# Performance work log

Hardware: AMD Instinct MI355X
Metric: run time of the kernel (lower is better)

Reference implementation:

```python
import jax, jax.numpy as jnp
import numpy as np

N = 50000      # nodes
K = 16         # out-degree before symmetrization
B = 8          # graphs in batch
H = 384        # hidden_channels
D = 64         # padded max neighbor slots per node (degree ~2K avg, Poisson tail << 64)
E = 2 * N * K  # directed edges after symmetrization


def setup_inputs() -> dict:
    key = jax.random.key(0)
    k1, k2, k3, k4, k5 = jax.random.split(key, 5)
    per = N // B
    rng = np.random.default_rng(0)
    src = np.repeat(np.arange(N, dtype=np.int32), K)
    # destinations stay inside the same graph block so clusters never cross graphs
    dst = ((src // per) * per + rng.integers(0, per, size=N * K)).astype(np.int32)
    ei = np.stack([np.concatenate([src, dst]), np.concatenate([dst, src])])
    edge_index = jnp.asarray(ei, dtype=jnp.int32)
    h = jax.random.normal(k1, (N, H), jnp.float32)
    edge_weight = jax.random.uniform(k2, (E,), jnp.float32)
    batch = jnp.asarray(np.arange(N) // per, dtype=jnp.int32)
    bound = 1.0 / np.sqrt(H)
    W_rel = jax.random.uniform(k3, (H, H), jnp.float32, -bound, bound)
    b_rel = jax.random.uniform(k4, (H,), jnp.float32, -bound, bound)
    W_root = jax.random.uniform(k5, (H, H), jnp.float32, -bound, bound)
    return dict(h=h, edge_index=edge_index, edge_weight=edge_weight, batch=batch,
                W_rel=W_rel, b_rel=b_rel, W_root=W_root)


def _graclus(edge_index, edge_weight, n):
    """Deterministic greedy weighted matching (graclus). Nodes processed in
    index order; an unmatched node grabs its max-weight unmatched neighbor.
    Returns cluster id per node (= index of the lower-id node of each pair)."""
    src, dst = edge_index[0], edge_index[1]
    e = src.shape[0]
    order = jnp.argsort(src)  # stable sort by source node
    s, d, w = src[order], dst[order], edge_weight[order]
    start = jnp.searchsorted(s, jnp.arange(n, dtype=s.dtype))  # first edge of each node
    pos = jnp.arange(e, dtype=s.dtype) - start[s]               # slot within node's list
    nbrs = jnp.full((n, D), -1, dtype=s.dtype).at[s, pos].set(d, mode='drop')
    wts = jnp.full((n, D), -jnp.inf, dtype=w.dtype).at[s, pos].set(w, mode='drop')

    def body(u, state):
        cluster, matched = state
        nb = nbrs[u]
        cand = (nb >= 0) & (nb != u) & (~matched[nb])
        wv = jnp.where(cand, wts[u], -jnp.inf)
        j = jnp.argmax(wv)
        can_match = cand[j] & (~matched[u])
        v = jnp.where(can_match, nb[j], u)
        cluster = cluster.at[v].set(jnp.where(can_match, u, cluster[v]))
        matched = matched.at[u].set(True).at[v].set(True)
        return cluster, matched

    cluster0 = jnp.arange(n, dtype=jnp.int32)
    matched0 = jnp.zeros(n, dtype=bool)
    cluster, _ = jax.lax.fori_loop(0, n, body, (cluster0, matched0))
    return cluster


def _forward(h, edge_index, edge_weight, batch, W_rel, b_rel, W_root):
    n = h.shape[0]
    cluster = _graclus(edge_index, edge_weight, n)
    # consecutive relabeling (PyG consecutive_cluster); padded to n clusters
    is_rep = jnp.zeros(n, bool).at[cluster].set(True)
    new_id = jnp.cumsum(is_rep.astype(jnp.int32)) - 1
    c = new_id[cluster]                       # [n] cluster id in [0, num_clusters)
    count = jax.ops.segment_sum(jnp.ones(n, jnp.float32), c, num_segments=n)
    nonempty = count > 0
    # max_pool node features
    x = jax.ops.segment_max(h, c, num_segments=n)
    x = jnp.where(nonempty[:, None], x, 0.0)
    # pooled batch vector
    b_pool = jax.ops.segment_max(batch, c, num_segments=n)
    b_pool = jnp.where(nonempty, b_pool, 0)
    # pool_edge: relabel, drop self-loops, coalesce duplicates
    cs, cd = c[edge_index[0]], c[edge_index[1]]
    order = jnp.lexsort((cd, cs))
    cs_s, cd_s = cs[order], cd[order]
    first = jnp.concatenate([jnp.ones(1, bool), (cs_s[1:] != cs_s[:-1]) | (cd_s[1:] != cd_s[:-1])])
    keep = first & (cs_s != cd_s)
    # GraphConv: out = lin_rel(sum_j x_j) + lin_root(x), then activation
    msg = jnp.where(keep[:, None], x[cs_s], 0.0)
    aggr = jax.ops.segment_sum(msg, cd_s, num_segments=n)
    out = jax.nn.relu(aggr @ W_rel.T + b_rel + x @ W_root.T)
    out = jnp.where(nonempty[:, None], out, 0.0)  # zero padded cluster rows
    return out, b_pool


def reference(h, edge_index, edge_weight, batch, W_rel, b_rel, W_root):
    return _forward(h, edge_index, edge_weight, batch, W_rel, b_rel, W_root)
```

## Files before the change

kernel.cpp:

```cpp
#include <hip/hip_runtime.h>
#include <math.h>

#define NN 50000
#define HH 384
#define KKC 16
#define PER 6250
#define EE 1600000
#define NKE 800000

#define OFF_NBRS   0UL
#define OFF_WTS    12800000UL
#define OFF_ADJ    0UL
#define OFF_CNT2   25600000UL
#define OFF_ADJC   25800000UL
#define OFF_CLUS   26000000UL
#define OFF_MATE   26200000UL
#define OFF_NEWID  26400000UL
#define OFF_CMAP   26600000UL
#define OFF_REPOF  26800000UL
#define OFF_NC     27000000UL
#define OFF_AGGR   27000256UL

__global__ void k0_init(int* cnt2, int* adjcnt) {
    int i = blockIdx.x * blockDim.x + threadIdx.x;
    if (i < NN) { cnt2[i] = 0; adjcnt[i] = 0; }
}

__global__ void k1_build(const int* __restrict__ ei, const float* __restrict__ ew,
                         int* __restrict__ nbrs, float* __restrict__ wts) {
    int id = blockIdx.x * blockDim.x + threadIdx.x;
    if (id >= NN * 64) return;
    int slot = id & 63;
    int u = id >> 6;
    if (slot < KKC) {
        int e = u * KKC + slot;
        nbrs[id] = ei[EE + e];
        wts[id]  = ew[e];
    } else {
        nbrs[id] = -1;
        wts[id]  = -INFINITY;
    }
}

__global__ void k2_scatter(const int* __restrict__ ei, int* __restrict__ cnt2,
                           int* __restrict__ nbrs) {
    int i = blockIdx.x * blockDim.x + threadIdx.x;
    if (i >= NKE) return;
    int u = ei[EE + i];
    int slot = atomicAdd(&cnt2[u], 1);
    if (slot < 48) nbrs[u * 64 + 16 + slot] = i;
}

__global__ __launch_bounds__(256) void k3_rank(const int* __restrict__ cnt2,
                                               const float* __restrict__ ew,
                                               int* __restrict__ nbrs,
                                               float* __restrict__ wts) {
    int gid = blockIdx.x * blockDim.x + threadIdx.x;
    int u = gid >> 6;
    int lane = gid & 63;
    if (u >= NN) return;
    int cnt = cnt2[u]; if (cnt > 48) cnt = 48;
    int myi = (lane < cnt) ? nbrs[u * 64 + 16 + lane] : 0x7FFFFFFF;
    int rank = 0;
    for (int m = 0; m < cnt; ++m) {
        int ov = __shfl(myi, m, 64);
        if (lane < cnt && m != lane && ov < myi) rank++;
    }
    if (lane < cnt) {
        nbrs[u * 64 + 16 + rank] = myi >> 4;
        wts [u * 64 + 16 + rank] = ew[NKE + myi];
    }
}

#define DPPMAX(x, ctrl) fmaxf((x), __int_as_float(__builtin_amdgcn_update_dpp( \
        (int)0xFF800000, __float_as_int(x), (ctrl), 0xf, 0xf, false)))

__device__ __forceinline__ void gstep(int u, int nl, float wt, unsigned gw, unsigned hw,
                                      int lane, unsigned* mbits, int* clus, int* mt,
                                      int& v1, int& v2, int& v3) {
    bool um = (((hw >> (u & 31)) & 1u) != 0u) || (u == v1) || (u == v2) || (u == v3);
    int vnew = -1;
    if (!um) {
        bool cand = (nl > u) && !((gw >> (nl & 31)) & 1u)
                    && (nl != v1) && (nl != v2) && (nl != v3);
        unsigned long long bal = __ballot(cand);
        if (bal) {
            float wv = cand ? wt : -INFINITY;
            float m = wv;
            m = DPPMAX(m, 0x111);
            m = DPPMAX(m, 0x112);
            m = DPPMAX(m, 0x114);
            m = DPPMAX(m, 0x118);
            m = DPPMAX(m, 0x142);
            m = DPPMAX(m, 0x143);
            float wmax = __int_as_float(__builtin_amdgcn_readlane(__float_as_int(m), 63));
            unsigned long long em = __ballot(cand && (wv == wmax));
            int j = (int)__builtin_ctzll(em);
            int vl = __builtin_amdgcn_readlane(nl, j);
            if (lane == 0) {
                atomicOr(&mbits[u  >> 5], 1u << (u  & 31));
                atomicOr(&mbits[vl >> 5], 1u << (vl & 31));
                mt[u] = vl; mt[vl] = u; clus[vl] = u;
            }
            vnew = vl;
        } else {
            if (lane == 0) atomicOr(&mbits[u >> 5], 1u << (u & 31));
        }
    }
    v3 = v2; v2 = v1; v1 = vnew;
}

__global__ __launch_bounds__(64) void k4_graclus(const int* __restrict__ nbrs,
                                                 const float* __restrict__ wts,
                                                 int* __restrict__ cluster,
                                                 int* __restrict__ mate) {
    __shared__ unsigned mbits[PER / 32 + 1];
    __shared__ int clus[PER];
    __shared__ int mt[PER];
    const int base = blockIdx.x * PER;
    const int lane = threadIdx.x;
    for (int i = lane; i < PER / 32 + 1; i += 64) mbits[i] = 0u;
    for (int i = lane; i < PER; i += 64) { clus[i] = i; mt[i] = -1; }
    __syncthreads();

    const int*   nrow = nbrs + (size_t)base * 64;
    const float* wrow = wts  + (size_t)base * 64;
    auto ldrow = [&](int r, int& nl, float& wt) {
        int rr = r < PER ? r : PER - 1;
        nl = nrow[(size_t)rr * 64 + lane] - base;
        wt = wrow[(size_t)rr * 64 + lane];
    };

    int   n0,n1,n2,n3, pb0,pb1,pb2,pb3, pc0,pc1,pc2,pc3;
    float w0,w1,w2,w3, qb0,qb1,qb2,qb3, qc0,qc1,qc2,qc3;
    ldrow(0,n0,w0);   ldrow(1,n1,w1);   ldrow(2,n2,w2);   ldrow(3,n3,w3);
    ldrow(4,pb0,qb0); ldrow(5,pb1,qb1); ldrow(6,pb2,qb2); ldrow(7,pb3,qb3);
    ldrow(8,pc0,qc0); ldrow(9,pc1,qc1); ldrow(10,pc2,qc2); ldrow(11,pc3,qc3);

    unsigned g0 = 0u, g1 = 0u, g2 = 0u, g3 = 0u;
    unsigned h0 = 0u, h1 = 0u, h2 = 0u, h3 = 0u;
    int v1 = -1, v2 = -1, v3 = -1;

    for (int u0 = 0; u0 < PER; u0 += 4) {
        gstep(u0 + 0, n0, w0, g0, h0, lane, mbits, clus, mt, v1, v2, v3);
        if (u0 + 1 < PER) gstep(u0 + 1, n1, w1, g1, h1, lane, mbits, clus, mt, v1, v2, v3);
        if (u0 + 2 < PER) gstep(u0 + 2, n2, w2, g2, h2, lane, mbits, clus, mt, v1, v2, v3);
        if (u0 + 3 < PER) gstep(u0 + 3, n3, w3, g3, h3, lane, mbits, clus, mt, v1, v2, v3);
        __builtin_amdgcn_sched_barrier(0);
        g0 = mbits[(pb0 < 0 ? 0 : pb0) >> 5];  h0 = mbits[(u0 + 4) >> 5];
        g1 = mbits[(pb1 < 0 ? 0 : pb1) >> 5];  h1 = mbits[(u0 + 5) >> 5];
        g2 = mbits[(pb2 < 0 ? 0 : pb2) >> 5];  h2 = mbits[(u0 + 6) >> 5];
        g3 = mbits[(pb3 < 0 ? 0 : pb3) >> 5];  h3 = mbits[(u0 + 7) >> 5];
        n0=pb0; w0=qb0; n1=pb1; w1=qb1; n2=pb2; w2=qb2; n3=pb3; w3=qb3;
        pb0=pc0; qb0=qc0; pb1=pc1; qb1=qc1; pb2=pc2; qb2=qc2; pb3=pc3; qb3=qc3;
        ldrow(u0+12, pc0, qc0); ldrow(u0+13, pc1, qc1);
        ldrow(u0+14, pc2, qc2); ldrow(u0+15, pc3, qc3);
    }
    __syncthreads();
    for (int i = lane; i < PER; i += 64) {
        cluster[base + i] = base + clus[i];
        int m = mt[i];
        mate[base + i] = (m < 0) ? -1 : base + m;
    }
}

__global__ __launch_bounds__(1024) void k5_scan(const int* __restrict__ cluster,
                                                int* __restrict__ newid,
                                                int* __restrict__ ncp) {
    __shared__ int wsum[16];
    __shared__ int carry;
    const int tid = threadIdx.x;
    const int lane = tid & 63;
    const int wid = tid >> 6;
    if (tid == 0) carry = 0;
    __syncthreads();
    for (int bse = 0; bse < NN; bse += 1024) {
        int u = bse + tid;
        int v = (u < NN && cluster[u] == u) ? 1 : 0;
        int s = v;
        #pragma unroll
        for (int off = 1; off < 64; off <<= 1) {
            int t = __shfl_up(s, off, 64);
            if (lane >= off) s += t;
        }
        if (lane == 63) wsum[wid] = s;
        __syncthreads();
        if (wid == 0) {
            int w2 = (lane < 16) ? wsum[lane] : 0;
            #pragma unroll
            for (int off = 1; off < 16; off <<= 1) {
                int t = __shfl_up(w2, off, 64);
                if (lane >= off) w2 += t;
            }
            if (lane < 16) wsum[lane] = w2;
        }
        __syncthreads();
        int wpre = (wid > 0) ? wsum[wid - 1] : 0;
        int carryv = carry;
        if (u < NN) newid[u] = carryv + wpre + s - 1;
        int total = wsum[15];
        __syncthreads();
        if (tid == 0) carry = carryv + total;
        __syncthreads();
    }
    if (tid == 0) *ncp = carry;
}

__global__ void k6_relabel(const int* __restrict__ cluster, const int* __restrict__ newid,
                           int* __restrict__ cmap, int* __restrict__ repof) {
    int u = blockIdx.x * blockDim.x + threadIdx.x;
    if (u >= NN) return;
    int cl = cluster[u];
    int cid = newid[cl];
    cmap[u] = cid;
    if (cl == u) repof[cid] = u;
}

__global__ __launch_bounds__(128) void k7_pool(const float* __restrict__ h,
                                               const int* __restrict__ repof,
                                               const int* __restrict__ mate,
                                               const int* __restrict__ batch,
                                               const int* __restrict__ ncp,
                                               float* __restrict__ xout,
                                               float* __restrict__ bpool) {
    int cid = blockIdx.x;
    int tid = threadIdx.x;
    int nc = *ncp;
    if (cid >= nc) {
        #pragma unroll
        for (int q = 0; q < 3; ++q) xout[(size_t)cid * HH + tid + q * 128] = 0.f;
        if (tid == 0) bpool[cid] = 0.f;
        return;
    }
    int u = repof[cid];
    int v = mate[u];
    const float* hu = h + (size_t)u * HH;
    const float* hv = h + (size_t)(v >= 0 ? v : u) * HH;
    #pragma unroll
    for (int q = 0; q < 3; ++q) {
        int j = tid + q * 128;
        float a = hu[j];
        if (v >= 0) a = fmaxf(a, hv[j]);
        xout[(size_t)cid * HH + j] = a;
    }
    if (tid == 0) bpool[cid] = (float)batch[u];
}

__global__ void k8_adj(const int* __restrict__ ei, const int* __restrict__ cmap,
                       int* __restrict__ adjcnt, int* __restrict__ adj) {
    int g = blockIdx.x * blockDim.x + threadIdx.x;
    if (g >= EE) return;
    int cs = cmap[ei[g]];
    int cd = cmap[ei[EE + g]];
    if (cs == cd) return;
    int slot = atomicAdd(&adjcnt[cd], 1);
    if (slot < 128) adj[(size_t)cd * 128 + slot] = cs;
}

__global__ __launch_bounds__(128) void k9_aggr(const int* __restrict__ adjcnt,
                                               const int* __restrict__ adj,
                                               const float* __restrict__ x,
                                               const int* __restrict__ ncp,
                                               float* __restrict__ aggr) {
    int cid = blockIdx.x;
    int tid = threadIdx.x;
    if (cid >= *ncp) return;
    int cnt = adjcnt[cid]; if (cnt > 128) cnt = 128;
    __shared__ int vals[128];
    __shared__ int keep[128];
    if (tid < cnt) vals[tid] = adj[(size_t)cid * 128 + tid];
    __syncthreads();
    if (tid < cnt) {
        int v = vals[tid]; int k = 1;
        for (int m = 0; m < tid; ++m) if (vals[m] == v) { k = 0; break; }
        keep[tid] = k;
    }
    __syncthreads();
    float a0 = 0.f, a1 = 0.f, a2 = 0.f;
    for (int e = 0; e < cnt; ++e) {
        if (keep[e]) {
            const float* xr = x + (size_t)vals[e] * HH;
            a0 += xr[tid]; a1 += xr[tid + 128]; a2 += xr[tid + 256];
        }
    }
    aggr[(size_t)cid * HH + tid]       = a0;
    aggr[(size_t)cid * HH + tid + 128] = a1;
    aggr[(size_t)cid * HH + tid + 256] = a2;
}

__global__ __launch_bounds__(256) void k10_gemm(const float* __restrict__ aggr,
                                                const float* __restrict__ h,
                                                const int* __restrict__ repof,
                                                const int* __restrict__ mate,
                                                const float* __restrict__ Wrel,
                                                const float* __restrict__ Wroot,
                                                const float* __restrict__ brel,
                                                float* __restrict__ out,
                                                const int* __restrict__ ncp) {
    const int nc = *ncp;
    const int row0 = blockIdx.x * 64;
    const int col0 = blockIdx.y * 64;
    if (row0 >= nc) return;
    __shared__ float As[32][68];
    __shared__ float Ws[32][68];
    __shared__ int us[64], vs[64];
    const int tid = threadIdx.x;
    if (tid < 64) {
        int r = row0 + tid;
        int u = 0, v = -1;
        if (r < nc) { u = repof[r]; v = mate[u]; }
        us[tid] = u; vs[tid] = v;
    }
    __syncthreads();
    float acc[4][4] = {};
    const int ty = tid >> 4, tx = tid & 15;
    for (int kt = 0; kt < 2 * HH; kt += 32) {
        #pragma unroll
        for (int q = 0; q < 2; ++q) {
            int idx = tid + q * 256;
            int r   = idx >> 3;
            int kq  = (idx & 7) << 2;
            int k   = kt + kq;
            int grow = row0 + r;
            bool rv = (grow < nc);
            float4 val;
            if (k < HH) {
                val = *(const float4*)(aggr + (size_t)(rv ? grow : 0) * HH + k);
            } else {
                int kk = k - HH;
                int u = us[r], v = vs[r];
                float4 a = *(const float4*)(h + (size_t)u * HH + kk);
                if (v >= 0) {
                    float4 b = *(const float4*)(h + (size_t)v * HH + kk);
                    a.x = fmaxf(a.x, b.x); a.y = fmaxf(a.y, b.y);
                    a.z = fmaxf(a.z, b.z); a.w = fmaxf(a.w, b.w);
                }
                val = a;
            }
            if (!rv) val = make_float4(0.f, 0.f, 0.f, 0.f);
            As[kq + 0][r] = val.x; As[kq + 1][r] = val.y;
            As[kq + 2][r] = val.z; As[kq + 3][r] = val.w;
        }
        {
            const float* Wsrc = (kt < HH) ? Wrel : Wroot;
            int kk0 = (kt < HH) ? kt : kt - HH;
            #pragma unroll
            for (int q = 0; q < 2; ++q) {
                int idx = tid + q * 256;
                int j   = idx >> 3;
                int kq  = (idx & 7) << 2;
                float4 w = *(const float4*)(Wsrc + (size_t)(col0 + j) * HH + kk0 + kq);
                Ws[kq + 0][j] = w.x; Ws[kq + 1][j] = w.y;
                Ws[kq + 2][j] = w.z; Ws[kq + 3][j] = w.w;
            }
        }
        __syncthreads();
        #pragma unroll
        for (int k = 0; k < 32; ++k) {
            float a[4], w[4];
            #pragma unroll
            for (int i = 0; i < 4; ++i) a[i] = As[k][ty * 4 + i];
            #pragma unroll
            for (int n = 0; n < 4; ++n) w[n] = Ws[k][tx * 4 + n];
            #pragma unroll
            for (int i = 0; i < 4; ++i)
                #pragma unroll
                for (int n = 0; n < 4; ++n)
                    acc[i][n] += a[i] * w[n];
        }
        __syncthreads();
    }
    #pragma unroll
    for (int i = 0; i < 4; ++i) {
        int r = row0 + ty * 4 + i;
        if (r >= nc) continue;
        #pragma unroll
        for (int n = 0; n < 4; ++n) {
            int j = col0 + tx * 4 + n;
            float v = acc[i][n] + brel[j];
            out[(size_t)r * HH + j] = v > 0.f ? v : 0.f;
        }
    }
}

extern "C" void kernel_launch(void* const* d_in, const int* in_sizes, int n_in,
                              void* d_out, int out_size, void* d_ws, size_t ws_size,
                              hipStream_t stream) {
    const float* h     = (const float*)d_in[0];
    const int*   ei    = (const int*)d_in[1];
    const float* ew    = (const float*)d_in[2];
    const int*   batch = (const int*)d_in[3];
    const float* Wrel  = (const float*)d_in[4];
    const float* brel  = (const float*)d_in[5];
    const float* Wroot = (const float*)d_in[6];
    float* out = (float*)d_out;

    unsigned char* w8 = (unsigned char*)d_ws;
    int*   nbrs   = (int*)(w8 + OFF_NBRS);
    float* wts    = (float*)(w8 + OFF_WTS);
    int*   adj    = (int*)(w8 + OFF_ADJ);
    int*   cnt2   = (int*)(w8 + OFF_CNT2);
    int*   adjcnt = (int*)(w8 + OFF_ADJC);
    int*   clus   = (int*)(w8 + OFF_CLUS);
    int*   mate   = (int*)(w8 + OFF_MATE);
    int*   newid  = (int*)(w8 + OFF_NEWID);
    int*   cmap   = (int*)(w8 + OFF_CMAP);
    int*   repof  = (int*)(w8 + OFF_REPOF);
    int*   ncp    = (int*)(w8 + OFF_NC);
    float* aggr   = (float*)(w8 + OFF_AGGR);

    float* xout  = out;
    float* bpool = out + (size_t)NN * HH;

    hipLaunchKernelGGL(k0_init,    dim3((NN + 255) / 256), dim3(256), 0, stream, cnt2, adjcnt);
    hipLaunchKernelGGL(k1_build,   dim3((NN * 64 + 255) / 256), dim3(256), 0, stream, ei, ew, nbrs, wts);
    hipLaunchKernelGGL(k2_scatter, dim3((NKE + 255) / 256), dim3(256), 0, stream, ei, cnt2, nbrs);
    hipLaunchKernelGGL(k3_rank,    dim3((NN * 64 + 255) / 256), dim3(256), 0, stream, cnt2, ew, nbrs, wts);
    hipLaunchKernelGGL(k4_graclus, dim3(8), dim3(64), 0, stream, nbrs, wts, clus, mate);
    hipLaunchKernelGGL(k5_scan,    dim3(1), dim3(1024), 0, stream, clus, newid, ncp);
    hipLaunchKernelGGL(k6_relabel, dim3((NN + 255) / 256), dim3(256), 0, stream, clus, newid, cmap, repof);
    hipLaunchKernelGGL(k7_pool,    dim3(NN), dim3(128), 0, stream, h, repof, mate, batch, ncp, xout, bpool);
    hipLaunchKernelGGL(k8_adj,     dim3((EE + 255) / 256), dim3(256), 0, stream, ei, cmap, adjcnt, adj);
    hipLaunchKernelGGL(k9_aggr,    dim3(NN), dim3(128), 0, stream, adjcnt, adj, xout, ncp, aggr);
    hipLaunchKernelGGL(k10_gemm,   dim3((NN + 63) / 64, HH / 64), dim3(256), 0, stream,
                       aggr, h, repof, mate, Wrel, Wroot, brel, out, ncp);
}
```

Before: 2.304 ms.

## Speculate graclus argmax ahead of commit and enlarge GEMM tiles

The serial graclus loop now computes each of the four nodes' argmax candidates speculatively before committing them in order. It redoes the reduction only when the speculative pick collides with a node matched in the previous three steps, which shortens the dependency chain per node. Separately, the fused GEMM goes from a 64x64 tile with 4x4 per thread to a 128x128 tile with 8x8 per thread and K-step 16, to raise arithmetic intensity. The larger tile increases register pressure and halves the K depth loaded per stage.

```diff
diff --git a/kernel.cpp b/kernel.cpp
--- a/kernel.cpp
+++ b/kernel.cpp
@@ -75,39 +75,15 @@
 #define DPPMAX(x, ctrl) fmaxf((x), __int_as_float(__builtin_amdgcn_update_dpp( \
         (int)0xFF800000, __float_as_int(x), (ctrl), 0xf, 0xf, false)))
 
-__device__ __forceinline__ void gstep(int u, int nl, float wt, unsigned gw, unsigned hw,
-                                      int lane, unsigned* mbits, int* clus, int* mt,
-                                      int& v1, int& v2, int& v3) {
-    bool um = (((hw >> (u & 31)) & 1u) != 0u) || (u == v1) || (u == v2) || (u == v3);
-    int vnew = -1;
-    if (!um) {
-        bool cand = (nl > u) && !((gw >> (nl & 31)) & 1u)
-                    && (nl != v1) && (nl != v2) && (nl != v3);
-        unsigned long long bal = __ballot(cand);
-        if (bal) {
-            float wv = cand ? wt : -INFINITY;
-            float m = wv;
-            m = DPPMAX(m, 0x111);
-            m = DPPMAX(m, 0x112);
-            m = DPPMAX(m, 0x114);
-            m = DPPMAX(m, 0x118);
-            m = DPPMAX(m, 0x142);
-            m = DPPMAX(m, 0x143);
-            float wmax = __int_as_float(__builtin_amdgcn_readlane(__float_as_int(m), 63));
-            unsigned long long em = __ballot(cand && (wv == wmax));
-            int j = (int)__builtin_ctzll(em);
-            int vl = __builtin_amdgcn_readlane(nl, j);
-            if (lane == 0) {
-                atomicOr(&mbits[u  >> 5], 1u << (u  & 31));
-                atomicOr(&mbits[vl >> 5], 1u << (vl & 31));
-                mt[u] = vl; mt[vl] = u; clus[vl] = u;
-            }
-            vnew = vl;
-        } else {
-            if (lane == 0) atomicOr(&mbits[u >> 5], 1u << (u & 31));
-        }
-    }
-    v3 = v2; v2 = v1; v1 = vnew;
+__device__ __forceinline__ float dpp_wavemax(float wv) {
+    float m = wv;
+    m = DPPMAX(m, 0x111);
+    m = DPPMAX(m, 0x112);
+    m = DPPMAX(m, 0x114);
+    m = DPPMAX(m, 0x118);
+    m = DPPMAX(m, 0x142);
+    m = DPPMAX(m, 0x143);
+    return __int_as_float(__builtin_amdgcn_readlane(__float_as_int(m), 63));
 }
 
 __global__ __launch_bounds__(64) void k4_graclus(const int* __restrict__ nbrs,
@@ -139,13 +115,54 @@
 
     unsigned g0 = 0u, g1 = 0u, g2 = 0u, g3 = 0u;
     unsigned h0 = 0u, h1 = 0u, h2 = 0u, h3 = 0u;
-    int v1 = -1, v2 = -1, v3 = -1;
+    int wA = -1, wB = -1, wC = -1;
+
+    auto specArg = [&](int u, int nl, float wt, unsigned gw,
+                       bool& candS, unsigned long long& em) -> int {
+        candS = (nl > u) && !((gw >> (nl & 31)) & 1u);
+        float wv = candS ? wt : -INFINITY;
+        float wmax = dpp_wavemax(wv);
+        em = __ballot(candS && (wv == wmax));
+        return em ? __builtin_amdgcn_readlane(nl, (int)__builtin_ctzll(em)) : -1;
+    };
+    auto commit = [&](int u, int nl, float wt, unsigned hw, bool candS, int vl) {
+        unsigned hword = (unsigned)__builtin_amdgcn_readfirstlane((int)hw);
+        bool um = (((hword >> (u & 31)) & 1u) != 0u) ||
+                  (u == wA) || (u == wB) || (u == wC);
+        int vnew = -1;
+        if (!um) {
+            if (vl >= 0 && (vl == wA || vl == wB || vl == wC)) {
+                bool cand = candS && (nl != wA) && (nl != wB) && (nl != wC);
+                float wv = cand ? wt : -INFINITY;
+                float wmax = dpp_wavemax(wv);
+                unsigned long long em2 = __ballot(cand && (wv == wmax));
+                vl = em2 ? __builtin_amdgcn_readlane(nl, (int)__builtin_ctzll(em2)) : -1;
+            }
+            if (vl >= 0) {
+                if (lane == 0) {
+                    atomicOr(&mbits[u  >> 5], 1u << (u  & 31));
+                    atomicOr(&mbits[vl >> 5], 1u << (vl & 31));
+                    mt[u] = vl; mt[vl] = u; clus[vl] = u;
+                }
+                vnew = vl;
+            } else {
+                if (lane == 0) atomicOr(&mbits[u >> 5], 1u << (u & 31));
+            }
+        }
+        wC = wB; wB = wA; wA = vnew;
+    };
 
     for (int u0 = 0; u0 < PER; u0 += 4) {
-        gstep(u0 + 0, n0, w0, g0, h0, lane, mbits, clus, mt, v1, v2, v3);
-        if (u0 + 1 < PER) gstep(u0 + 1, n1, w1, g1, h1, lane, mbits, clus, mt, v1, v2, v3);
-        if (u0 + 2 < PER) gstep(u0 + 2, n2, w2, g2, h2, lane, mbits, clus, mt, v1, v2, v3);
-        if (u0 + 3 < PER) gstep(u0 + 3, n3, w3, g3, h3, lane, mbits, clus, mt, v1, v2, v3);
+        bool c0, c1, c2, c3;
+        unsigned long long e0, e1, e2, e3;
+        int vl0 = specArg(u0 + 0, n0, w0, g0, c0, e0);
+        int vl1 = specArg(u0 + 1, n1, w1, g1, c1, e1);
+        int vl2 = specArg(u0 + 2, n2, w2, g2, c2, e2);
+        int vl3 = specArg(u0 + 3, n3, w3, g3, c3, e3);
+        commit(u0 + 0, n0, w0, h0, c0, vl0);
+        if (u0 + 1 < PER) commit(u0 + 1, n1, w1, h1, c1, vl1);
+        if (u0 + 2 < PER) commit(u0 + 2, n2, w2, h2, c2, vl2);
+        if (u0 + 3 < PER) commit(u0 + 3, n3, w3, h3, c3, vl3);
         __builtin_amdgcn_sched_barrier(0);
         g0 = mbits[(pb0 < 0 ? 0 : pb0) >> 5];  h0 = mbits[(u0 + 4) >> 5];
         g1 = mbits[(pb1 < 0 ? 0 : pb1) >> 5];  h1 = mbits[(u0 + 5) >> 5];
@@ -298,31 +315,31 @@
                                                 float* __restrict__ out,
                                                 const int* __restrict__ ncp) {
     const int nc = *ncp;
-    const int row0 = blockIdx.x * 64;
-    const int col0 = blockIdx.y * 64;
+    const int row0 = blockIdx.x * 128;
+    const int col0 = blockIdx.y * 128;
     if (row0 >= nc) return;
-    __shared__ float As[32][68];
-    __shared__ float Ws[32][68];
-    __shared__ int us[64], vs[64];
+    __shared__ float As[16][132];
+    __shared__ float Ws[16][132];
+    __shared__ int us[128], vs[128];
     const int tid = threadIdx.x;
-    if (tid < 64) {
+    if (tid < 128) {
         int r = row0 + tid;
         int u = 0, v = -1;
         if (r < nc) { u = repof[r]; v = mate[u]; }
         us[tid] = u; vs[tid] = v;
     }
     __syncthreads();
-    float acc[4][4] = {};
+    float acc[8][8] = {};
     const int ty = tid >> 4, tx = tid & 15;
-    for (int kt = 0; kt < 2 * HH; kt += 32) {
+    for (int kt = 0; kt < 2 * HH; kt += 16) {
         #pragma unroll
         for (int q = 0; q < 2; ++q) {
-            int idx = tid + q * 256;
-            int r   = idx >> 3;
-            int kq  = (idx & 7) << 2;
-            int k   = kt + kq;
+            int flat = tid + q * 256;
+            int r    = flat >> 2;
+            int kq   = (flat & 3) << 2;
+            int k    = kt + kq;
             int grow = row0 + r;
-            bool rv = (grow < nc);
+            bool rv  = (grow < nc);
             float4 val;
             if (k < HH) {
                 val = *(const float4*)(aggr + (size_t)(rv ? grow : 0) * HH + k);
@@ -346,9 +363,9 @@
             int kk0 = (kt < HH) ? kt : kt - HH;
             #pragma unroll
             for (int q = 0; q < 2; ++q) {
-                int idx = tid + q * 256;
-                int j   = idx >> 3;
-                int kq  = (idx & 7) << 2;
+                int flat = tid + q * 256;
+                int j    = flat >> 2;
+                int kq   = (flat & 3) << 2;
                 float4 w = *(const float4*)(Wsrc + (size_t)(col0 + j) * HH + kk0 + kq);
                 Ws[kq + 0][j] = w.x; Ws[kq + 1][j] = w.y;
                 Ws[kq + 2][j] = w.z; Ws[kq + 3][j] = w.w;
@@ -356,27 +373,27 @@
         }
         __syncthreads();
         #pragma unroll
-        for (int k = 0; k < 32; ++k) {
-            float a[4], w[4];
+        for (int k = 0; k < 16; ++k) {
+            float a[8], w[8];
             #pragma unroll
-            for (int i = 0; i < 4; ++i) a[i] = As[k][ty * 4 + i];
+            for (int i = 0; i < 8; ++i) a[i] = As[k][ty * 8 + i];
             #pragma unroll
-            for (int n = 0; n < 4; ++n) w[n] = Ws[k][tx * 4 + n];
+            for (int n = 0; n < 8; ++n) w[n] = Ws[k][tx * 8 + n];
             #pragma unroll
-            for (int i = 0; i < 4; ++i)
+            for (int i = 0; i < 8; ++i)
                 #pragma unroll
-                for (int n = 0; n < 4; ++n)
+                for (int n = 0; n < 8; ++n)
                     acc[i][n] += a[i] * w[n];
         }
         __syncthreads();
     }
     #pragma unroll
-    for (int i = 0; i < 4; ++i) {
-        int r = row0 + ty * 4 + i;
+    for (int i = 0; i < 8; ++i) {
+        int r = row0 + ty * 8 + i;
         if (r >= nc) continue;
         #pragma unroll
-        for (int n = 0; n < 4; ++n) {
-            int j = col0 + tx * 4 + n;
+        for (int n = 0; n < 8; ++n) {
+            int j = col0 + tx * 8 + n;
             float v = acc[i][n] + brel[j];
             out[(size_t)r * HH + j] = v > 0.f ? v : 0.f;
         }
@@ -422,6 +439,6 @@
     hipLaunchKernelGGL(k7_pool,    dim3(NN), dim3(128), 0, stream, h, repof, mate, batch, ncp, xout, bpool);
     hipLaunchKernelGGL(k8_adj,     dim3((EE + 255) / 256), dim3(256), 0, stream, ei, cmap, adjcnt, adj);
     hipLaunchKernelGGL(k9_aggr,    dim3(NN), dim3(128), 0, stream, adjcnt, adj, xout, ncp, aggr);
-    hipLaunchKernelGGL(k10_gemm,   dim3((NN + 63) / 64, HH / 64), dim3(256), 0, stream,
+    hipLaunchKernelGGL(k10_gemm,   dim3((NN + 127) / 128, HH / 128), dim3(256), 0, stream,
                        aggr, h, repof, mate, Wrel, Wroot, brel, out, ncp);
 }
```

Measured after the change: 2.812 ms. 1.22x slower.
